# Performance work log

Measured on AMD Instinct MI355X. Metric: run time of the kernel, lower is better.

The kernel has to match this reference:

```python
import jax, jax.numpy as jnp
import numpy as np

EMBED = 1024
HEADS = 16
HEAD_DIM = EMBED // HEADS


def setup_inputs() -> dict:
    key = jax.random.key(0)
    ks = jax.random.split(key, 8)
    N, L = 2, 2048
    s = 0.02
    return {
        "values": jax.random.normal(ks[0], (N, L, EMBED), jnp.float32),
        "keys": jax.random.normal(ks[1], (N, L, EMBED), jnp.float32),
        "queries": jax.random.normal(ks[2], (N, L, EMBED), jnp.float32),
        # per-head projection weights, SHARED across heads (nn.Linear(head_dim, head_dim))
        "Wv": jax.random.normal(ks[3], (HEAD_DIM, HEAD_DIM), jnp.float32) * s,
        "Wk": jax.random.normal(ks[4], (HEAD_DIM, HEAD_DIM), jnp.float32) * s,
        "Wq": jax.random.normal(ks[5], (HEAD_DIM, HEAD_DIM), jnp.float32) * s,
        "Wo": jax.random.normal(ks[6], (EMBED, EMBED), jnp.float32) * s,
        "bo": jax.random.normal(ks[7], (EMBED,), jnp.float32) * s,
    }


def reference(values, keys, queries, Wv, Wk, Wq, Wo, bo):
    N, Lq, _ = queries.shape
    Lk = keys.shape[1]
    Lv = values.shape[1]
    # split heads: (N, L, H, D)
    v = values.reshape(N, Lv, HEADS, HEAD_DIM)
    k = keys.reshape(N, Lk, HEADS, HEAD_DIM)
    q = queries.reshape(N, Lq, HEADS, HEAD_DIM)
    # per-head linear (weight shared across heads); nn.Linear computes x @ W.T
    v = jnp.einsum('nlhd,ed->nlhe', v, Wv)
    k = jnp.einsum('nlhd,ed->nlhe', k, Wk)
    q = jnp.einsum('nlhd,ed->nlhe', q, Wq)
    # scores (N, H, Lq, Lk); NOTE: scale uses sqrt(embed_size), as in the original
    scores = jnp.einsum('nqhd,nkhd->nhqk', q, k) / jnp.sqrt(jnp.float32(EMBED))
    attn = jax.nn.softmax(scores, axis=-1)
    out = jnp.einsum('nhql,nlhd->nqhd', attn, v).reshape(N, Lq, EMBED)
    out = out @ Wo.T + bo
    return out
```

## Files before the change

### kernel.cpp

```cpp
#include <hip/hip_runtime.h>
#include <hip/hip_bf16.h>

#define EMBED 1024
#define HEADS 16
#define HD 64
#define NB 2
#define LSEQ 2048

typedef __bf16 bf16x8 __attribute__((ext_vector_type(8)));
typedef float f32x4 __attribute__((ext_vector_type(4)));

static __device__ __forceinline__ __bf16 f2b(float x) {
    union { __hip_bfloat16 h; __bf16 b; } u;
    u.h = __float2bfloat16(x);
    return u.b;
}
static __device__ __forceinline__ bf16x8 cvt8(float4 a, float4 b) {
    bf16x8 r;
    r[0] = f2b(a.x); r[1] = f2b(a.y); r[2] = f2b(a.z); r[3] = f2b(a.w);
    r[4] = f2b(b.x); r[5] = f2b(b.y); r[6] = f2b(b.z); r[7] = f2b(b.w);
    return r;
}
static __device__ __forceinline__ unsigned short b2u(float x) {
    union { __hip_bfloat16 h; unsigned short u; } c;
    c.h = __float2bfloat16(x);
    return c.u;
}

#define GLD16(g, l) __builtin_amdgcn_global_load_lds( \
    (const __attribute__((address_space(1))) void*)(g), \
    (__attribute__((address_space(3))) void*)(l), 16, 0, 0)


__global__ __launch_bounds__(256) void proj_kernel(
    const float* __restrict__ vals,
    const float* __restrict__ keys,
    const float* __restrict__ quer,
    const float* __restrict__ Wv,
    const float* __restrict__ Wk,
    const float* __restrict__ Wq,
    const float* __restrict__ Wo,
    __hip_bfloat16* __restrict__ QF,
    __hip_bfloat16* __restrict__ KF,
    __hip_bfloat16* __restrict__ VF,
    __hip_bfloat16* __restrict__ Wob)
{
    if (blockIdx.x >= 1536) {
        int base = ((blockIdx.x - 1536) * 256 + threadIdx.x) * 16;
#pragma unroll
        for (int j = 0; j < 16; j += 4) {
            float4 w4 = *(const float4*)(Wo + base + j);
            __hip_bfloat16 o[4] = {
                __float2bfloat16(w4.x), __float2bfloat16(w4.y),
                __float2bfloat16(w4.z), __float2bfloat16(w4.w)};
            *(ushort4*)(Wob + base + j) = *(const ushort4*)o;
        }
        return;
    }

    int b      = blockIdx.x;
    int tensor = b % 3;
    int rem    = b / 3;
    int n      = rem >> 8;
    int lt     = (rem >> 3) & 31;
    int hp     = rem & 7;
    int t = threadIdx.x, w = t >> 6, lane = t & 63;
    int m16 = lane & 15, quad = lane >> 4;
    int l0 = lt * 64 + w * 16;

    const float* X = (tensor == 0) ? quer : (tensor == 1 ? keys : vals);
    const float* W = (tensor == 0) ? Wq   : (tensor == 1 ? Wk   : Wv);
    float scale = (tensor == 0) ? (1.44269504088896340736f / 32.0f) : 1.0f;

    const float* xb = X + ((size_t)n * LSEQ + l0 + m16) * EMBED + (hp * 2) * HD + quad * 8;
    bf16x8 xf[2][2];
#pragma unroll
    for (int hh = 0; hh < 2; ++hh)
#pragma unroll
        for (int kk = 0; kk < 2; ++kk) {
            const float* xp = xb + hh * HD + kk * 32;
            xf[hh][kk] = cvt8(*(const float4*)xp, *(const float4*)(xp + 4));
        }

    bf16x8 wf[4][2];
#pragma unroll
    for (int f = 0; f < 4; ++f)
#pragma unroll
        for (int kk = 0; kk < 2; ++kk) {
            const float* wp = W + (f * 16 + m16) * HD + kk * 32 + quad * 8;
            wf[f][kk] = cvt8(*(const float4*)wp, *(const float4*)(wp + 4));
        }

#pragma unroll
    for (int hh = 0; hh < 2; ++hh) {
        int h = hp * 2 + hh;
        size_t nhb = (size_t)(n * HEADS + h) * 131072;
        if (tensor != 2) {
            f32x4 acc[4] = {};
#pragma unroll
            for (int f = 0; f < 4; ++f) {
                acc[f] = __builtin_amdgcn_mfma_f32_16x16x32_bf16(wf[f][0], xf[hh][0], acc[f], 0, 0, 0);
                acc[f] = __builtin_amdgcn_mfma_f32_16x16x32_bf16(wf[f][1], xf[hh][1], acc[f], 0, 0, 0);
            }
            int key = l0 + m16;
#pragma unroll
            for (int f = 0; f < 4; ++f) {
                union { ushort4 u; unsigned short s[4]; } p;
#pragma unroll
                for (int r = 0; r < 4; ++r) p.s[r] = b2u(acc[f][r] * scale);
                int kk   = f >> 1;
                int qk2  = (f & 1) * 2 + (quad >> 1);
                int j4   = (quad & 1) * 4;
                __hip_bfloat16* dst;
                if (tensor == 0) {
                    dst = QF + nhb + (size_t)(l0 >> 4) * 1024 + kk * 512
                        + (qk2 * 16 + m16) * 8 + j4;
                } else {
                    dst = KF + nhb + (size_t)(key >> 5) * 2048
                        + ((key & 1) * 2 + kk) * 512
                        + (qk2 * 16 + ((key & 31) >> 1)) * 8 + j4;
                }
                *(ushort4*)dst = p.u;
            }
        } else {
            f32x4 acc[4] = {};
#pragma unroll
            for (int f = 0; f < 4; ++f) {
                acc[f] = __builtin_amdgcn_mfma_f32_16x16x32_bf16(xf[hh][0], wf[f][0], acc[f], 0, 0, 0);
                acc[f] = __builtin_amdgcn_mfma_f32_16x16x32_bf16(xf[hh][1], wf[f][1], acc[f], 0, 0, 0);
            }
            int keyq  = l0 + quad * 4;
            int c     = keyq >> 5;
            int quadv = (keyq & 31) >> 3;
            int j4    = (quad & 1) * 4;
#pragma unroll
            for (int f = 0; f < 4; ++f) {
                union { ushort4 u; unsigned short s[4]; } p;
#pragma unroll
                for (int r = 0; r < 4; ++r) p.s[r] = b2u(acc[f][r]);
                __hip_bfloat16* dst = VF + nhb + (size_t)c * 2048 + f * 512
                    + quadv * 128 + m16 * 8 + j4;
                *(ushort4*)dst = p.u;
            }
        }
    }
}

#define CHUNKS 32

#define LOADK(KFR, c_) do { \
    const __hip_bfloat16* kc_ = kp + (size_t)(c_) * 2048; \
    KFR[0][0] = *(const bf16x8*)(kc_); \
    KFR[0][1] = *(const bf16x8*)(kc_ + 512); \
    KFR[1][0] = *(const bf16x8*)(kc_ + 1024); \
    KFR[1][1] = *(const bf16x8*)(kc_ + 1536); \
} while (0)

#define LOADV(c_) do { \
    const __hip_bfloat16* vc_ = vp + (size_t)(c_) * 2048; \
    vf[0] = *(const bf16x8*)(vc_); \
    vf[1] = *(const bf16x8*)(vc_ + 512); \
    vf[2] = *(const bf16x8*)(vc_ + 1024); \
    vf[3] = *(const bf16x8*)(vc_ + 1536); \
} while (0)

#define SCOREX(KFR, PF) do { \
    f32x4 s_[2][2]; \
    __builtin_amdgcn_s_setprio(1); \
    _Pragma("unroll") \
    for (int tq_ = 0; tq_ < 2; ++tq_) { \
        _Pragma("unroll") \
        for (int t2_ = 0; t2_ < 2; ++t2_) { \
            f32x4 z_; \
            z_ = __builtin_amdgcn_mfma_f32_16x16x32_bf16(KFR[t2_][0], qf[tq_][0], zf, 0, 0, 0); \
            z_ = __builtin_amdgcn_mfma_f32_16x16x32_bf16(KFR[t2_][1], qf[tq_][1], z_, 0, 0, 0); \
            s_[tq_][t2_] = z_; \
        } \
    } \
    __builtin_amdgcn_s_setprio(0); \
    _Pragma("unroll") \
    for (int tq_ = 0; tq_ < 2; ++tq_) { \
        _Pragma("unroll") \
        for (int r_ = 0; r_ < 4; ++r_) { \
            PF[tq_][2 * r_]     = f2b(__builtin_amdgcn_exp2f(s_[tq_][0][r_])); \
            PF[tq_][2 * r_ + 1] = f2b(__builtin_amdgcn_exp2f(s_[tq_][1][r_])); \
        } \
    } \
} while (0)

#define PVX(PF) do { \
    __builtin_amdgcn_s_setprio(1); \
    _Pragma("unroll") \
    for (int f_ = 0; f_ < 4; ++f_) { \
        of[0][f_] = __builtin_amdgcn_mfma_f32_16x16x32_bf16(vf[f_], PF[0], of[0][f_], 0, 0, 0); \
        of[1][f_] = __builtin_amdgcn_mfma_f32_16x16x32_bf16(vf[f_], PF[1], of[1][f_], 0, 0, 0); \
    } \
    lsa[0] = __builtin_amdgcn_mfma_f32_16x16x32_bf16(onesf, PF[0], lsa[0], 0, 0, 0); \
    lsa[1] = __builtin_amdgcn_mfma_f32_16x16x32_bf16(onesf, PF[1], lsa[1], 0, 0, 0); \
    __builtin_amdgcn_s_setprio(0); \
} while (0)

__global__ __launch_bounds__(256) void attn_kernel(
    const __hip_bfloat16* __restrict__ QF,
    const __hip_bfloat16* __restrict__ KF,
    const __hip_bfloat16* __restrict__ VF,
    __hip_bfloat16* __restrict__ AO)
{
    __shared__ __align__(16) float Cb[5120];

    int i  = blockIdx.x;
    int x  = i & 7, r2 = i >> 3;
    int nh = x * 4 + (r2 >> 5);
    int qblk = r2 & 31;

    int t = threadIdx.x, w = t >> 6, lane = t & 63;
    int m16 = lane & 15, quad = lane >> 4;
    int qh = w & 1, kh = w >> 1;
    int q0 = qblk * 64 + qh * 32;
    size_t nhb = (size_t)nh * 131072;

    const __hip_bfloat16* qb = QF + nhb + (size_t)(q0 >> 4) * 1024 + lane * 8;
    bf16x8 qf[2][2];
#pragma unroll
    for (int tq = 0; tq < 2; ++tq)
#pragma unroll
        for (int kk = 0; kk < 2; ++kk)
            qf[tq][kk] = *(const bf16x8*)(qb + tq * 1024 + kk * 512);

    const __hip_bfloat16* kp = KF + nhb + (size_t)(kh * 32) * 2048 + lane * 8;
    const __hip_bfloat16* vp = VF + nhb + (size_t)(kh * 32) * 2048 + lane * 8;

    bf16x8 onesf;
#pragma unroll
    for (int j = 0; j < 8; ++j) onesf[j] = f2b(1.0f);
    const f32x4 zf = {};

    f32x4 of[2][4] = {};
    f32x4 lsa[2] = {};
    bf16x8 ka[2][2], kb[2][2], vf[4], pA[2], pB[2];

    LOADK(ka, 0);
    LOADK(kb, 1);
    SCOREX(ka, pA);
    LOADV(0);

#pragma unroll 1
    for (int tt = 0; tt < 15; ++tt) {
        int c = 2 * tt;
        LOADK(ka, c + 2);
        SCOREX(kb, pB);
        PVX(pA);
        LOADV(c + 1);
        LOADK(kb, c + 3);
        SCOREX(ka, pA);
        PVX(pB);
        LOADV(c + 2);
    }
    SCOREX(kb, pB);
    PVX(pA);
    LOADV(31);
    PVX(pB);

    __syncthreads();
    if (kh == 1) {
        int base = qh * 2560;
#pragma unroll
        for (int tq = 0; tq < 2; ++tq)
#pragma unroll
            for (int f = 0; f < 4; ++f)
                *(f32x4*)&Cb[base + (tq * 4 + f) * 256 + lane * 4] = of[tq][f];
#pragma unroll
        for (int tq = 0; tq < 2; ++tq)
            Cb[base + 2048 + tq * 64 + lane] = lsa[tq][0];
    }
    __syncthreads();
    if (kh == 0) {
        int base = qh * 2560;
#pragma unroll
        for (int tq = 0; tq < 2; ++tq)
#pragma unroll
            for (int f = 0; f < 4; ++f)
                of[tq][f] += *(const f32x4*)&Cb[base + (tq * 4 + f) * 256 + lane * 4];
        int n = nh >> 4, h = nh & 15;
#pragma unroll
        for (int tq = 0; tq < 2; ++tq) {
            float lt2 = lsa[tq][0] + Cb[base + 2048 + tq * 64 + lane];
            float rinv = 1.0f / lt2;
            int qrow = q0 + tq * 16 + m16;
#pragma unroll
            for (int f = 0; f < 4; ++f) {
                union { ushort4 u; unsigned short s[4]; } pk;
#pragma unroll
                for (int r = 0; r < 4; ++r) pk.s[r] = b2u(of[tq][f][r] * rinv);
                int col = h * HD + f * 16 + quad * 4;
                *(ushort4*)&AO[((size_t)n * LSEQ + qrow) * EMBED + col] = pk.u;
            }
        }
    }
}

__global__ __launch_bounds__(256) void outproj_kernel(
    const __hip_bfloat16* __restrict__ AO,
    const __hip_bfloat16* __restrict__ Wob,
    const float* __restrict__ bo,
    float* __restrict__ out)
{
    __shared__ __align__(16) __hip_bfloat16 As[2][2][64][32];
    __shared__ __align__(16) __hip_bfloat16 Bs[2][2][64][32];

    int b  = blockIdx.x;
    int wk = (b & 7) * 128 + (b >> 3);
    int mt = wk >> 4, nt = wk & 15;
    int m0 = mt * 64, n0 = nt * 64;
    int t = threadIdx.x, w = t >> 6, lane = t & 63;
    int m16 = lane & 15, quad = lane >> 4;

    int srow = lane >> 2;
    int scol = (lane & 3) * 8;

    const __hip_bfloat16* Ab = AO  + (size_t)m0 * EMBED;
    const __hip_bfloat16* Bb = Wob + (size_t)n0 * EMBED;

#define STAGE_OP(bb, k0_) do { \
    GLD16(Ab + (size_t)(w * 16 + srow) * EMBED + (k0_) +      scol, &As[bb][0][w * 16][0]); \
    GLD16(Ab + (size_t)(w * 16 + srow) * EMBED + (k0_) + 32 + scol, &As[bb][1][w * 16][0]); \
    GLD16(Bb + (size_t)(w * 16 + srow) * EMBED + (k0_) +      scol, &Bs[bb][0][w * 16][0]); \
    GLD16(Bb + (size_t)(w * 16 + srow) * EMBED + (k0_) + 32 + scol, &Bs[bb][1][w * 16][0]); \
} while (0)

    f32x4 acc[4] = {};
    STAGE_OP(0, 0);

#pragma unroll 1
    for (int ks = 0; ks < 16; ++ks) {
        int cur = ks & 1;
        if (ks < 15) {
            STAGE_OP(cur ^ 1, (ks + 1) * 64);
            asm volatile("s_waitcnt vmcnt(4)" ::: "memory");
        } else {
            asm volatile("s_waitcnt vmcnt(0)" ::: "memory");
        }
        __builtin_amdgcn_s_barrier();

        bf16x8 af[2], bfr[2][4];
#pragma unroll
        for (int kk = 0; kk < 2; ++kk)
            af[kk] = *(const bf16x8*)&As[cur][kk][w * 16 + m16][quad * 8];
#pragma unroll
        for (int kk = 0; kk < 2; ++kk)
#pragma unroll
            for (int tb = 0; tb < 4; ++tb)
                bfr[kk][tb] = *(const bf16x8*)&Bs[cur][kk][tb * 16 + m16][quad * 8];
        asm volatile("s_waitcnt lgkmcnt(0)" ::: "memory");
        __builtin_amdgcn_s_barrier();

#pragma unroll
        for (int tb = 0; tb < 4; ++tb) {
            acc[tb] = __builtin_amdgcn_mfma_f32_16x16x32_bf16(af[0], bfr[0][tb], acc[tb], 0, 0, 0);
            acc[tb] = __builtin_amdgcn_mfma_f32_16x16x32_bf16(af[1], bfr[1][tb], acc[tb], 0, 0, 0);
        }
    }

#pragma unroll
    for (int tb = 0; tb < 4; ++tb) {
        int col = n0 + tb * 16 + m16;
        float bias = bo[col];
#pragma unroll
        for (int r = 0; r < 4; ++r) {
            int row = m0 + w * 16 + quad * 4 + r;
            out[(size_t)row * EMBED + col] = acc[tb][r] + bias;
        }
    }
#undef STAGE_OP
}

extern "C" void kernel_launch(void* const* d_in, const int* in_sizes, int n_in,
                              void* d_out, int out_size, void* d_ws, size_t ws_size,
                              hipStream_t stream) {
    const float* vals = (const float*)d_in[0];
    const float* keys = (const float*)d_in[1];
    const float* quer = (const float*)d_in[2];
    const float* Wv   = (const float*)d_in[3];
    const float* Wk   = (const float*)d_in[4];
    const float* Wq   = (const float*)d_in[5];
    const float* Wo   = (const float*)d_in[6];
    const float* bo   = (const float*)d_in[7];
    float* out = (float*)d_out;

    __hip_bfloat16* ws = (__hip_bfloat16*)d_ws;
    const size_t PE = (size_t)NB * HEADS * LSEQ * HD;
    __hip_bfloat16* QF  = ws;
    __hip_bfloat16* KF  = ws + PE;
    __hip_bfloat16* VF  = ws + 2 * PE;
    __hip_bfloat16* AO  = ws + 3 * PE;
    __hip_bfloat16* Wob = ws + 4 * PE;

    proj_kernel<<<1536 + 256, 256, 0, stream>>>(
        vals, keys, quer, Wv, Wk, Wq, Wo, QF, KF, VF, Wob);
    attn_kernel<<<1024, 256, 0, stream>>>(QF, KF, VF, AO);
    outproj_kernel<<<1024, 256, 0, stream>>>(AO, Wob, bo, out);
}
```

Measured before the change: 168.5 us.

## Stage K/V chunks through double-buffered LDS with direct global-to-LDS loads

Rather than each wave loading its own K and V fragments from global memory into registers, the four waves now cooperatively stage K and V chunks into a double-buffered shared-memory area using direct global-to-LDS loads. Each wave then reads its fragments from LDS, with waitcnt and barriers ordering the stages. The goal is to cut redundant global traffic, since waves sharing a key half previously loaded the same K/V, and to overlap the next chunk's fetch with compute. The cost is two block barriers per chunk plus LDS read latency inside the main loop, and the pipeline depth drops from the earlier register-level software pipelining.

```diff
diff --git a/kernel.cpp b/kernel.cpp
--- a/kernel.cpp
+++ b/kernel.cpp
@@ -146,22 +146,26 @@
     }
 }
 
-#define CHUNKS 32
-
-#define LOADK(KFR, c_) do { \
-    const __hip_bfloat16* kc_ = kp + (size_t)(c_) * 2048; \
-    KFR[0][0] = *(const bf16x8*)(kc_); \
-    KFR[0][1] = *(const bf16x8*)(kc_ + 512); \
-    KFR[1][0] = *(const bf16x8*)(kc_ + 1024); \
-    KFR[1][1] = *(const bf16x8*)(kc_ + 1536); \
-} while (0)
-
-#define LOADV(c_) do { \
-    const __hip_bfloat16* vc_ = vp + (size_t)(c_) * 2048; \
-    vf[0] = *(const bf16x8*)(vc_); \
-    vf[1] = *(const bf16x8*)(vc_ + 512); \
-    vf[2] = *(const bf16x8*)(vc_ + 1024); \
-    vf[3] = *(const bf16x8*)(vc_ + 1536); \
+
+#define STAGE(b_, c_) do { \
+    const __hip_bfloat16* s_ = gsrc + (size_t)(c_) * 2048; \
+    GLD16(s_,        &SB[b_][wst]); \
+    GLD16(s_ +  512, &SB[b_][wst + 1024]); \
+    GLD16(s_ + 1024, &SB[b_][wst + 2048]); \
+    GLD16(s_ + 1536, &SB[b_][wst + 3072]); \
+} while (0)
+
+#define READKV(b_, VR) do { \
+    const __hip_bfloat16* kb_ = (const __hip_bfloat16*)&SB[b_][kh * 4096 + lane * 16]; \
+    kreg[0][0] = *(const bf16x8*)(kb_); \
+    kreg[0][1] = *(const bf16x8*)(kb_ + 512); \
+    kreg[1][0] = *(const bf16x8*)(kb_ + 1024); \
+    kreg[1][1] = *(const bf16x8*)(kb_ + 1536); \
+    const __hip_bfloat16* vb_ = kb_ + 4096; \
+    VR[0] = *(const bf16x8*)(vb_); \
+    VR[1] = *(const bf16x8*)(vb_ + 512); \
+    VR[2] = *(const bf16x8*)(vb_ + 1024); \
+    VR[3] = *(const bf16x8*)(vb_ + 1536); \
 } while (0)
 
 #define SCOREX(KFR, PF) do { \
@@ -188,16 +192,28 @@
     } \
 } while (0)
 
-#define PVX(PF) do { \
+#define PVX(PF, VFR) do { \
     __builtin_amdgcn_s_setprio(1); \
     _Pragma("unroll") \
     for (int f_ = 0; f_ < 4; ++f_) { \
-        of[0][f_] = __builtin_amdgcn_mfma_f32_16x16x32_bf16(vf[f_], PF[0], of[0][f_], 0, 0, 0); \
-        of[1][f_] = __builtin_amdgcn_mfma_f32_16x16x32_bf16(vf[f_], PF[1], of[1][f_], 0, 0, 0); \
+        of[0][f_] = __builtin_amdgcn_mfma_f32_16x16x32_bf16(VFR[f_], PF[0], of[0][f_], 0, 0, 0); \
+        of[1][f_] = __builtin_amdgcn_mfma_f32_16x16x32_bf16(VFR[f_], PF[1], of[1][f_], 0, 0, 0); \
     } \
     lsa[0] = __builtin_amdgcn_mfma_f32_16x16x32_bf16(onesf, PF[0], lsa[0], 0, 0, 0); \
     lsa[1] = __builtin_amdgcn_mfma_f32_16x16x32_bf16(onesf, PF[1], lsa[1], 0, 0, 0); \
     __builtin_amdgcn_s_setprio(0); \
+} while (0)
+
+#define ITER(b_, c_, VN, VP) do { \
+    STAGE((b_) ^ 1, (c_) + 1); \
+    asm volatile("s_waitcnt vmcnt(4)" ::: "memory"); \
+    __builtin_amdgcn_s_barrier(); \
+    READKV(b_, VN); \
+    PVX(pP, VP); \
+    __builtin_amdgcn_sched_barrier(0); \
+    asm volatile("s_waitcnt lgkmcnt(0)" ::: "memory"); \
+    __builtin_amdgcn_s_barrier(); \
+    SCOREX(kreg, pP); \
 } while (0)
 
 __global__ __launch_bounds__(256) void attn_kernel(
@@ -206,7 +222,7 @@
     const __hip_bfloat16* __restrict__ VF,
     __hip_bfloat16* __restrict__ AO)
 {
-    __shared__ __align__(16) float Cb[5120];
+    __shared__ __align__(16) unsigned char SB[2][16384];
 
     int i  = blockIdx.x;
     int x  = i & 7, r2 = i >> 3;
@@ -227,8 +243,9 @@
         for (int kk = 0; kk < 2; ++kk)
             qf[tq][kk] = *(const bf16x8*)(qb + tq * 1024 + kk * 512);
 
-    const __hip_bfloat16* kp = KF + nhb + (size_t)(kh * 32) * 2048 + lane * 8;
-    const __hip_bfloat16* vp = VF + nhb + (size_t)(kh * 32) * 2048 + lane * 8;
+    const __hip_bfloat16* gsrc = (w < 2 ? KF : VF) + nhb
+        + (size_t)((w & 1) * 32) * 2048 + (size_t)lane * 8;
+    int wst = w * 4096;
 
     bf16x8 onesf;
 #pragma unroll
@@ -237,30 +254,36 @@
 
     f32x4 of[2][4] = {};
     f32x4 lsa[2] = {};
-    bf16x8 ka[2][2], kb[2][2], vf[4], pA[2], pB[2];
-
-    LOADK(ka, 0);
-    LOADK(kb, 1);
-    SCOREX(ka, pA);
-    LOADV(0);
+    bf16x8 kreg[2][2], vA[4], vB[4], pP[2];
+
+    STAGE(0, 0);
+    asm volatile("s_waitcnt vmcnt(0)" ::: "memory");
+    __builtin_amdgcn_s_barrier();
+
+    STAGE(1, 1);
+    asm volatile("s_waitcnt vmcnt(4)" ::: "memory");
+    __builtin_amdgcn_s_barrier();
+    READKV(0, vA);
+    __builtin_amdgcn_sched_barrier(0);
+    asm volatile("s_waitcnt lgkmcnt(0)" ::: "memory");
+    __builtin_amdgcn_s_barrier();
+    SCOREX(kreg, pP);
 
 #pragma unroll 1
     for (int tt = 0; tt < 15; ++tt) {
-        int c = 2 * tt;
-        LOADK(ka, c + 2);
-        SCOREX(kb, pB);
-        PVX(pA);
-        LOADV(c + 1);
-        LOADK(kb, c + 3);
-        SCOREX(ka, pA);
-        PVX(pB);
-        LOADV(c + 2);
-    }
-    SCOREX(kb, pB);
-    PVX(pA);
-    LOADV(31);
-    PVX(pB);
-
+        ITER(1, 2 * tt + 1, vB, vA);
+        ITER(0, 2 * tt + 2, vA, vB);
+    }
+    asm volatile("s_waitcnt vmcnt(0)" ::: "memory");
+    __builtin_amdgcn_s_barrier();
+    READKV(1, vB);
+    PVX(pP, vA);
+    __builtin_amdgcn_sched_barrier(0);
+    asm volatile("s_waitcnt lgkmcnt(0)" ::: "memory");
+    SCOREX(kreg, pP);
+    PVX(pP, vB);
+
+    float* Cb = (float*)&SB[0][0];
     __syncthreads();
     if (kh == 1) {
         int base = qh * 2560;
```

Measured after the change: 171.3 us. No clear change (+1.6%).
